# Kernel optimization log

Hardware: AMD Instinct MI355X
Metric: run time of the kernel (lower is better)

## Reference

```python
import jax, jax.numpy as jnp
import numpy as np

B, A, C = 8, 150000, 10
ALPHA, GAMMA = 0.25, 2.0
STD = jnp.array([[0.1, 0.1, 0.2, 0.2]], dtype=jnp.float32)


def setup_inputs() -> dict:
    key = jax.random.key(0)
    ks = jax.random.split(key, 9)
    # ground-truth boxes (one per image), centered around (400,400)
    cx = jax.random.uniform(ks[0], (B,), minval=350., maxval=450.)
    cy = jax.random.uniform(ks[1], (B,), minval=350., maxval=450.)
    w = jax.random.uniform(ks[2], (B,), minval=80., maxval=180.)
    h = jax.random.uniform(ks[3], (B,), minval=80., maxval=180.)
    boxes = jnp.stack([cx - 0.5 * w, cy - 0.5 * h, cx + 0.5 * w, cy + 0.5 * h], axis=1)
    labels = (jax.random.uniform(ks[4], (B, C)) < 0.3).astype(jnp.float32)
    annotations = jnp.concatenate([boxes, labels], axis=1)  # [B, 4+C]
    n_near = A // 20
    kc = jax.random.split(ks[5], 4)
    ncx = jax.random.uniform(kc[0], (n_near,), minval=350., maxval=450.)
    ncy = jax.random.uniform(kc[1], (n_near,), minval=350., maxval=450.)
    nw = jax.random.uniform(kc[2], (n_near,), minval=80., maxval=180.)
    nh = jax.random.uniform(kc[3], (n_near,), minval=80., maxval=180.)
    kr = jax.random.split(ks[6], 4)
    rcx = jax.random.uniform(kr[0], (A - n_near,), minval=0., maxval=800.)
    rcy = jax.random.uniform(kr[1], (A - n_near,), minval=0., maxval=800.)
    rw = jax.random.uniform(kr[2], (A - n_near,), minval=20., maxval=300.)
    rh = jax.random.uniform(kr[3], (A - n_near,), minval=20., maxval=300.)
    acx = jnp.concatenate([ncx, rcx]); acy = jnp.concatenate([ncy, rcy])
    aw = jnp.concatenate([nw, rw]); ah = jnp.concatenate([nh, rh])
    anchors = jnp.stack([acx - 0.5 * aw, acy - 0.5 * ah, acx + 0.5 * aw, acy + 0.5 * ah], axis=1)[None]  # [1,A,4]
    attributes = jax.random.uniform(ks[7], (B, A, C), dtype=jnp.float32)  # probs in (0,1)
    regressions = jax.random.normal(ks[8], (B, A, 4), dtype=jnp.float32)
    return {"attributes": attributes, "regressions": regressions,
            "anchors": anchors, "annotations": annotations}


def reference(attributes, regressions, anchors, annotations):
    anchor = anchors[0]  # [A,4]
    aw = anchor[:, 2] - anchor[:, 0]
    ah = anchor[:, 3] - anchor[:, 1]
    acx = anchor[:, 0] + 0.5 * aw
    acy = anchor[:, 1] + 0.5 * ah

    def per_image(attribute, regression, ann):  # [A,C], [A,4], [4+C]
        box, labels = ann[:4], ann[4:]
        attribute = jnp.clip(attribute, 1e-4, 1.0 - 1e-4)
        # IoU of every anchor with the single gt box -> [A]
        area = (box[2] - box[0]) * (box[3] - box[1])
        iw = jnp.clip(jnp.minimum(anchor[:, 2], box[2]) - jnp.maximum(anchor[:, 0], box[0]), 0.0)
        ih = jnp.clip(jnp.minimum(anchor[:, 3], box[3]) - jnp.maximum(anchor[:, 1], box[1]), 0.0)
        inter = iw * ih
        union = jnp.clip(aw * ah + area - inter, 1e-8)
        iou = inter / union
        neg = iou < 0.4
        pos = iou >= 0.5
        num_pos = pos.sum()
        # classification targets: -1 ignore, 0 background, gt labels for positives
        targets = jnp.full(attribute.shape, -1.0, attribute.dtype)
        targets = jnp.where(neg[:, None], 0.0, targets)
        targets = jnp.where(pos[:, None], labels[None, :], targets)
        alpha_factor = jnp.where(targets == 1.0, ALPHA, 1.0 - ALPHA)
        focal_w = jnp.where(targets == 1.0, 1.0 - attribute, attribute)
        focal_w = alpha_factor * focal_w ** GAMMA
        bce = -(targets * jnp.log(attribute) + (1.0 - targets) * jnp.log(1.0 - attribute))
        att_loss = jnp.where(targets != -1.0, focal_w * bce, 0.0)
        att_loss = att_loss.sum() / jnp.maximum(num_pos.astype(attribute.dtype), 1.0)
        gw_raw = box[2] - box[0]; gh_raw = box[3] - box[1]
        gcx = box[0] + 0.5 * gw_raw; gcy = box[1] + 0.5 * gh_raw
        gw = jnp.clip(gw_raw, 1.0); gh = jnp.clip(gh_raw, 1.0)
        t = jnp.stack([(gcx - acx) / aw, (gcy - acy) / ah,
                       jnp.log(gw / aw), jnp.log(gh / ah)], axis=1) / STD  # [A,4]
        diff = jnp.abs(t - regression)
        rl = jnp.where(diff <= 1.0 / 9.0, 0.5 * 9.0 * diff ** 2, diff - 0.5 / 9.0)
        rl_sum = jnp.where(pos[:, None], rl, 0.0).sum()
        denom = jnp.maximum(num_pos, 1).astype(attribute.dtype) * 4.0  # mean over [P,4]
        reg_loss = jnp.where(num_pos > 0, rl_sum / denom, 0.0)
        return att_loss, reg_loss

    att_losses, reg_losses = jax.vmap(per_image)(attributes, regressions, annotations)
    return (att_losses.mean(keepdims=True), reg_losses.mean(keepdims=True))
```

## Files before the change

kernel.cpp:

```cpp
#include <hip/hip_runtime.h>

constexpr int B_IMG = 8;
constexpr int A_ANCH = 150000;
constexpr int C_CLS = 10;
constexpr int TPB = 256;
constexpr int APT = 4;
constexpr int NBX = (A_ANCH + TPB * APT - 1) / (TPB * APT);

__global__ __launch_bounds__(TPB) void focal_main(
    const float* __restrict__ attr,
    const float* __restrict__ regr,
    const float* __restrict__ anch,
    const float* __restrict__ ann,
    float* __restrict__ att_part,
    float* __restrict__ rl_part,
    float* __restrict__ np_part)
{
    const int b = blockIdx.y;
    const int a0 = (blockIdx.x * TPB + threadIdx.x) * APT;
    const bool valid = (a0 < A_ANCH);

    float4 at4[10];
    float4 an4[4];
    if (valid) {
        const float4* ap = reinterpret_cast<const float4*>(attr + ((size_t)b * A_ANCH + a0) * C_CLS);
#pragma unroll
        for (int j = 0; j < 10; ++j) at4[j] = ap[j];
        const float4* anp = reinterpret_cast<const float4*>(anch) + a0;
#pragma unroll
        for (int j = 0; j < 4; ++j) an4[j] = anp[j];
    }

    const float* annb = ann + b * 14;
    const float bx0 = annb[0], by0 = annb[1], bx1 = annb[2], by1 = annb[3];
    float lab[C_CLS];
#pragma unroll
    for (int c = 0; c < C_CLS; ++c) lab[c] = annb[4 + c];

    const float gw_raw = bx1 - bx0;
    const float gh_raw = by1 - by0;
    const float area = gw_raw * gh_raw;
    const float gcx = bx0 + 0.5f * gw_raw;
    const float gcy = by0 + 0.5f * gh_raw;
    const float gw = fmaxf(gw_raw, 1.0f);
    const float gh = fmaxf(gh_raw, 1.0f);

    const float TH  = (float)(1.0 / 9.0);
    const float SUB = (float)(0.5 / 9.0);
    const float PHI = (float)(1.0 - 0.0001);

    float att_sum = 0.0f;
    float rl_sum = 0.0f;
    int np = 0;

    if (valid) {
        float av[4 * C_CLS];
#pragma unroll
        for (int j = 0; j < 10; ++j) {
            av[4 * j + 0] = at4[j].x;
            av[4 * j + 1] = at4[j].y;
            av[4 * j + 2] = at4[j].z;
            av[4 * j + 3] = at4[j].w;
        }

#pragma unroll
        for (int k = 0; k < APT; ++k) {
            const float ax0 = an4[k].x, ay0 = an4[k].y, ax1 = an4[k].z, ay1 = an4[k].w;
            const float aw = ax1 - ax0;
            const float ah = ay1 - ay0;
            float iw = fminf(ax1, bx1) - fmaxf(ax0, bx0);
            float ih = fminf(ay1, by1) - fmaxf(ay0, by0);
            iw = fmaxf(iw, 0.0f);
            ih = fmaxf(ih, 0.0f);
            const float inter = iw * ih;
            const float uni = fmaxf(aw * ah + area - inter, 1e-8f);
            const float iou = inter / uni;
            const bool pos = (iou >= 0.5f);
            const bool neg = (iou < 0.4f);

            if (pos || neg) {
#pragma unroll
                for (int c = 0; c < C_CLS; ++c) {
                    float p = av[k * C_CLS + c];
                    p = fminf(fmaxf(p, 1e-4f), PHI);
                    const float tgt = pos ? lab[c] : 0.0f;
                    float loss;
                    if (tgt == 1.0f) {
                        const float q = 1.0f - p;
                        loss = 0.25f * (q * q) * (-logf(p));
                    } else {
                        loss = 0.75f * (p * p) * (-logf(1.0f - p));
                    }
                    att_sum += loss;
                }
            }
            if (pos) {
                ++np;
                const float acx = ax0 + 0.5f * aw;
                const float acy = ay0 + 0.5f * ah;
                const float t0 = ((gcx - acx) / aw) / 0.1f;
                const float t1 = ((gcy - acy) / ah) / 0.1f;
                const float t2 = logf(gw / aw) / 0.2f;
                const float t3 = logf(gh / ah) / 0.2f;
                const float4 r = *reinterpret_cast<const float4*>(regr + ((size_t)b * A_ANCH + a0 + k) * 4);
                float d;
                d = fabsf(t0 - r.x); rl_sum += (d <= TH) ? 4.5f * d * d : d - SUB;
                d = fabsf(t1 - r.y); rl_sum += (d <= TH) ? 4.5f * d * d : d - SUB;
                d = fabsf(t2 - r.z); rl_sum += (d <= TH) ? 4.5f * d * d : d - SUB;
                d = fabsf(t3 - r.w); rl_sum += (d <= TH) ? 4.5f * d * d : d - SUB;
            }
        }
    }

    float npf = (float)np;
#pragma unroll
    for (int off = 32; off > 0; off >>= 1) {
        att_sum += __shfl_down(att_sum, off);
        rl_sum  += __shfl_down(rl_sum, off);
        npf     += __shfl_down(npf, off);
    }

    __shared__ float s_att[TPB / 64];
    __shared__ float s_rl[TPB / 64];
    __shared__ float s_np[TPB / 64];
    const int wave = threadIdx.x >> 6;
    const int lane = threadIdx.x & 63;
    if (lane == 0) { s_att[wave] = att_sum; s_rl[wave] = rl_sum; s_np[wave] = npf; }
    __syncthreads();
    if (threadIdx.x == 0) {
        float a0s = 0.0f, r0 = 0.0f, n0 = 0.0f;
#pragma unroll
        for (int w = 0; w < TPB / 64; ++w) { a0s += s_att[w]; r0 += s_rl[w]; n0 += s_np[w]; }
        const int idx = b * NBX + blockIdx.x;
        att_part[idx] = a0s;
        rl_part[idx]  = r0;
        np_part[idx]  = n0;
    }
}

__global__ __launch_bounds__(512) void focal_finalize(
    const float* __restrict__ att_part,
    const float* __restrict__ rl_part,
    const float* __restrict__ np_part,
    float* __restrict__ out)
{
    const int wave = threadIdx.x >> 6;
    const int lane = threadIdx.x & 63;
    float as = 0.0f, rs = 0.0f, ns = 0.0f;
    if (wave < B_IMG) {
        for (int i = lane; i < NBX; i += 64) {
            as += att_part[wave * NBX + i];
            rs += rl_part[wave * NBX + i];
            ns += np_part[wave * NBX + i];
        }
    }
#pragma unroll
    for (int off = 32; off > 0; off >>= 1) {
        as += __shfl_down(as, off);
        rs += __shfl_down(rs, off);
        ns += __shfl_down(ns, off);
    }
    __shared__ float sa[B_IMG], sr[B_IMG], sn[B_IMG];
    if (lane == 0 && wave < B_IMG) { sa[wave] = as; sr[wave] = rs; sn[wave] = ns; }
    __syncthreads();
    if (threadIdx.x == 0) {
        double am = 0.0, rm = 0.0;
        for (int b = 0; b < B_IMG; ++b) {
            const double npd = (double)sn[b];
            const double npf = npd > 0.0 ? npd : 1.0;
            am += (double)sa[b] / npf;
            if (npd > 0.0) rm += (double)sr[b] / (npf * 4.0);
        }
        out[0] = (float)(am / (double)B_IMG);
        out[1] = (float)(rm / (double)B_IMG);
    }
}

extern "C" void kernel_launch(void* const* d_in, const int* in_sizes, int n_in,
                              void* d_out, int out_size, void* d_ws, size_t ws_size,
                              hipStream_t stream) {
    const float* attr = (const float*)d_in[0];
    const float* regr = (const float*)d_in[1];
    const float* anch = (const float*)d_in[2];
    const float* ann  = (const float*)d_in[3];
    float* out = (float*)d_out;

    float* att_part = (float*)d_ws;
    float* rl_part  = att_part + B_IMG * NBX;
    float* np_part  = rl_part + B_IMG * NBX;

    dim3 grid(NBX, B_IMG);
    focal_main<<<grid, TPB, 0, stream>>>(attr, regr, anch, ann, att_part, rl_part, np_part);
    focal_finalize<<<1, 512, 0, stream>>>(att_part, rl_part, np_part, out);
}
```

Measured before the change: 25.53 us.

## Stage attributes through LDS with coalesced loads and add wave-level negative fast path

Each block now loads its attribute tile with fully coalesced float4 reads and transposes it into shared memory class-major, so each thread handles two anchors instead of four. This replaces the old per-thread strided 160-byte loads. It also adds a wave-uniform fast path that uses only the negative-class loss when no anchor in the wave is positive. In exchange it adds a shared-memory transpose with mod/div indexing, likely bank conflicts on the scattered stores, a __syncthreads, and twice as many blocks.

After: 24.89 us. -2.5%, faster.

```diff
diff --git a/kernel.cpp b/kernel.cpp
--- a/kernel.cpp
+++ b/kernel.cpp
@@ -4,8 +4,11 @@
 constexpr int A_ANCH = 150000;
 constexpr int C_CLS = 10;
 constexpr int TPB = 256;
-constexpr int APT = 4;
-constexpr int NBX = (A_ANCH + TPB * APT - 1) / (TPB * APT);
+constexpr int BA = TPB * 2;
+constexpr int NBX = (A_ANCH + BA - 1) / BA;
+constexpr int F4_PER_IMG = A_ANCH * C_CLS / 4;
+constexpr int F4_PER_BLK = BA * C_CLS / 4;
+constexpr int FLT_PER_BLK = BA * C_CLS;
 
 __global__ __launch_bounds__(TPB) void focal_main(
     const float* __restrict__ attr,
@@ -16,19 +19,38 @@
     float* __restrict__ rl_part,
     float* __restrict__ np_part)
 {
+    __shared__ float sAttr[C_CLS * BA];
+
     const int b = blockIdx.y;
-    const int a0 = (blockIdx.x * TPB + threadIdx.x) * APT;
+    const int tid = threadIdx.x;
+
+    {
+        const float4* ap = reinterpret_cast<const float4*>(attr) + (size_t)b * F4_PER_IMG;
+        const int blkF4 = blockIdx.x * F4_PER_BLK;
+#pragma unroll
+        for (int j = 0; j < 5; ++j) {
+            int f4 = blkF4 + j * TPB + tid;
+            f4 = (f4 < F4_PER_IMG) ? f4 : (F4_PER_IMG - 1);
+            const float4 v = ap[f4];
+            const unsigned l0 = (unsigned)(f4 * 4 - blockIdx.x * FLT_PER_BLK);
+            const float vv[4] = {v.x, v.y, v.z, v.w};
+#pragma unroll
+            for (int d = 0; d < 4; ++d) {
+                const unsigned l = l0 + d;
+                sAttr[(l % 10u) * BA + (l / 10u)] = vv[d];
+            }
+        }
+    }
+
+    const int a0 = blockIdx.x * BA + tid * 2;
     const bool valid = (a0 < A_ANCH);
 
-    float4 at4[10];
-    float4 an4[4];
+    float4 anA = make_float4(0.f, 0.f, 0.f, 0.f);
+    float4 anB = anA;
     if (valid) {
-        const float4* ap = reinterpret_cast<const float4*>(attr + ((size_t)b * A_ANCH + a0) * C_CLS);
-#pragma unroll
-        for (int j = 0; j < 10; ++j) at4[j] = ap[j];
         const float4* anp = reinterpret_cast<const float4*>(anch) + a0;
-#pragma unroll
-        for (int j = 0; j < 4; ++j) an4[j] = anp[j];
+        anA = anp[0];
+        anB = anp[1];
     }
 
     const float* annb = ann + b * 14;
@@ -49,59 +71,86 @@
     const float SUB = (float)(0.5 / 9.0);
     const float PHI = (float)(1.0 - 0.0001);
 
+    __syncthreads();
+
     float att_sum = 0.0f;
     float rl_sum = 0.0f;
-    int np = 0;
+    float npf = 0.0f;
 
     if (valid) {
-        float av[4 * C_CLS];
-#pragma unroll
-        for (int j = 0; j < 10; ++j) {
-            av[4 * j + 0] = at4[j].x;
-            av[4 * j + 1] = at4[j].y;
-            av[4 * j + 2] = at4[j].z;
-            av[4 * j + 3] = at4[j].w;
-        }
-
-#pragma unroll
-        for (int k = 0; k < APT; ++k) {
-            const float ax0 = an4[k].x, ay0 = an4[k].y, ax1 = an4[k].z, ay1 = an4[k].w;
-            const float aw = ax1 - ax0;
-            const float ah = ay1 - ay0;
-            float iw = fminf(ax1, bx1) - fmaxf(ax0, bx0);
-            float ih = fminf(ay1, by1) - fmaxf(ay0, by0);
+        bool pos[2], neg[2];
+        float aw[2], ah[2], ax0v[2], ay0v[2];
+        const float4 an[2] = {anA, anB};
+#pragma unroll
+        for (int k = 0; k < 2; ++k) {
+            ax0v[k] = an[k].x; ay0v[k] = an[k].y;
+            aw[k] = an[k].z - an[k].x;
+            ah[k] = an[k].w - an[k].y;
+            float iw = fminf(an[k].z, bx1) - fmaxf(an[k].x, bx0);
+            float ih = fminf(an[k].w, by1) - fmaxf(an[k].y, by0);
             iw = fmaxf(iw, 0.0f);
             ih = fmaxf(ih, 0.0f);
             const float inter = iw * ih;
-            const float uni = fmaxf(aw * ah + area - inter, 1e-8f);
+            const float uni = fmaxf(aw[k] * ah[k] + area - inter, 1e-8f);
             const float iou = inter / uni;
-            const bool pos = (iou >= 0.5f);
-            const bool neg = (iou < 0.4f);
-
-            if (pos || neg) {
+            pos[k] = (iou >= 0.5f);
+            neg[k] = (iou < 0.4f);
+        }
+        const bool act0 = pos[0] || neg[0];
+        const bool act1 = pos[1] || neg[1];
+        const bool wave_has_pos = __any(pos[0] || pos[1]);
+
+        const float2* row = reinterpret_cast<const float2*>(sAttr) + tid;
+
+        if (act0 || act1) {
+            if (!wave_has_pos) {
 #pragma unroll
                 for (int c = 0; c < C_CLS; ++c) {
-                    float p = av[k * C_CLS + c];
-                    p = fminf(fmaxf(p, 1e-4f), PHI);
-                    const float tgt = pos ? lab[c] : 0.0f;
-                    float loss;
-                    if (tgt == 1.0f) {
-                        const float q = 1.0f - p;
-                        loss = 0.25f * (q * q) * (-logf(p));
-                    } else {
-                        loss = 0.75f * (p * p) * (-logf(1.0f - p));
+                    const float2 pv = row[c * (BA / 2)];
+                    if (act0) {
+                        const float p = fminf(fmaxf(pv.x, 1e-4f), PHI);
+                        att_sum += 0.75f * p * p * (-logf(1.0f - p));
                     }
-                    att_sum += loss;
+                    if (act1) {
+                        const float p = fminf(fmaxf(pv.y, 1e-4f), PHI);
+                        att_sum += 0.75f * p * p * (-logf(1.0f - p));
+                    }
+                }
+            } else {
+#pragma unroll
+                for (int c = 0; c < C_CLS; ++c) {
+                    const float2 pv = row[c * (BA / 2)];
+                    const float pp[2] = {pv.x, pv.y};
+#pragma unroll
+                    for (int k = 0; k < 2; ++k) {
+                        const bool act = k ? act1 : act0;
+                        if (act) {
+                            const float p = fminf(fmaxf(pp[k], 1e-4f), PHI);
+                            const float tgt = pos[k] ? lab[c] : 0.0f;
+                            float loss;
+                            if (tgt == 1.0f) {
+                                const float q = 1.0f - p;
+                                loss = 0.25f * (q * q) * (-logf(p));
+                            } else {
+                                loss = 0.75f * (p * p) * (-logf(1.0f - p));
+                            }
+                            att_sum += loss;
+                        }
+                    }
                 }
             }
-            if (pos) {
-                ++np;
-                const float acx = ax0 + 0.5f * aw;
-                const float acy = ay0 + 0.5f * ah;
-                const float t0 = ((gcx - acx) / aw) / 0.1f;
-                const float t1 = ((gcy - acy) / ah) / 0.1f;
-                const float t2 = logf(gw / aw) / 0.2f;
-                const float t3 = logf(gh / ah) / 0.2f;
+        }
+
+#pragma unroll
+        for (int k = 0; k < 2; ++k) {
+            if (pos[k]) {
+                npf += 1.0f;
+                const float acx = ax0v[k] + 0.5f * aw[k];
+                const float acy = ay0v[k] + 0.5f * ah[k];
+                const float t0 = ((gcx - acx) / aw[k]) / 0.1f;
+                const float t1 = ((gcy - acy) / ah[k]) / 0.1f;
+                const float t2 = logf(gw / aw[k]) / 0.2f;
+                const float t3 = logf(gh / ah[k]) / 0.2f;
                 const float4 r = *reinterpret_cast<const float4*>(regr + ((size_t)b * A_ANCH + a0 + k) * 4);
                 float d;
                 d = fabsf(t0 - r.x); rl_sum += (d <= TH) ? 4.5f * d * d : d - SUB;
@@ -112,7 +161,6 @@
         }
     }
 
-    float npf = (float)np;
 #pragma unroll
     for (int off = 32; off > 0; off >>= 1) {
         att_sum += __shfl_down(att_sum, off);
@@ -123,11 +171,11 @@
     __shared__ float s_att[TPB / 64];
     __shared__ float s_rl[TPB / 64];
     __shared__ float s_np[TPB / 64];
-    const int wave = threadIdx.x >> 6;
-    const int lane = threadIdx.x & 63;
+    const int wave = tid >> 6;
+    const int lane = tid & 63;
     if (lane == 0) { s_att[wave] = att_sum; s_rl[wave] = rl_sum; s_np[wave] = npf; }
     __syncthreads();
-    if (threadIdx.x == 0) {
+    if (tid == 0) {
         float a0s = 0.0f, r0 = 0.0f, n0 = 0.0f;
 #pragma unroll
         for (int w = 0; w < TPB / 64; ++w) { a0s += s_att[w]; r0 += s_rl[w]; n0 += s_np[w]; }
```
